# Kernel tuning notes

Measured on AMD Instinct MI355X. Metric: run time of the kernel, lower is better.

## Reference

```python
import jax, jax.numpy as jnp
import numpy as np

N_HEAD, D_MODEL, D_K, D_V = 16, 1024, 64, 64
BIAS_WEIGHT = 1.0
NEG = -10000.0


def setup_inputs() -> dict:
    key = jax.random.key(0)
    ks = jax.random.split(key, 9)
    B, L = 2, 2048
    q = jax.random.normal(ks[0], (B, L, D_MODEL), dtype=jnp.float32)
    k = jax.random.normal(ks[1], (B, L, D_MODEL), dtype=jnp.float32)
    v = jax.random.normal(ks[2], (B, L, D_MODEL), dtype=jnp.float32)
    mask = jax.random.randint(ks[3], (B, L, L), 0, 2, dtype=jnp.int32)
    bias = jax.random.normal(ks[4], (B, L, L), dtype=jnp.float32)
    s = 1.0 / np.sqrt(D_MODEL)
    w_qs = jax.random.uniform(ks[5], (D_MODEL, N_HEAD * D_K), jnp.float32, -s, s)
    w_ks = jax.random.uniform(ks[6], (D_MODEL, N_HEAD * D_K), jnp.float32, -s, s)
    w_vs = jax.random.uniform(ks[7], (D_MODEL, N_HEAD * D_V), jnp.float32, -s, s)
    w_fc = jax.random.uniform(ks[8], (N_HEAD * D_V, D_MODEL), jnp.float32, -s, s)
    return {"q": q, "k": k, "v": v, "mask": mask, "bias": bias,
            "w_qs": w_qs, "w_ks": w_ks, "w_vs": w_vs, "w_fc": w_fc}


def reference(q, k, v, mask, bias, w_qs, w_ks, w_vs, w_fc):
    B, Lq, _ = q.shape
    # project and split heads: [B, H, L, d]
    qh = (q @ w_qs).reshape(B, Lq, N_HEAD, D_K).transpose(0, 2, 1, 3)
    kh = (k @ w_ks).reshape(B, k.shape[1], N_HEAD, D_K).transpose(0, 2, 1, 3)
    vh = (v @ w_vs).reshape(B, v.shape[1], N_HEAD, D_V).transpose(0, 2, 1, 3)
    temperature = D_K ** 0.5
    attn = jnp.einsum('bhqd,bhkd->bhqk', qh / temperature, kh)
    attn = attn + bias[:, None, :, :] * BIAS_WEIGHT
    attn = jnp.where(mask[:, None, :, :] == 0, NEG, attn)
    attn = jax.nn.softmax(attn, axis=-1)
    out = jnp.einsum('bhqk,bhkd->bhqd', attn, vh)
    out = out.transpose(0, 2, 1, 3).reshape(B, Lq, N_HEAD * D_V)
    return out @ w_fc
```

## Files before the change

kernel.cpp:

```cpp
#include <hip/hip_runtime.h>
#include <cstddef>

#define DEV static __device__ __forceinline__

typedef float f32x4 __attribute__((ext_vector_type(4)));
typedef __bf16 bf16x8 __attribute__((ext_vector_type(8)));
typedef __bf16 bf16x4v __attribute__((ext_vector_type(4)));
typedef unsigned short u16x8 __attribute__((ext_vector_type(8)));
typedef unsigned short u16x4 __attribute__((ext_vector_type(4)));
typedef unsigned u32x2 __attribute__((ext_vector_type(2)));
typedef unsigned u32x4 __attribute__((ext_vector_type(4)));
typedef _Float16 f16;
typedef _Float16 f16x4 __attribute__((ext_vector_type(4)));

constexpr int BB = 2, LL = 2048, DM = 1024, NH = 16, DK = 64;
constexpr float LOG2E = 1.44269504f;

DEV unsigned short f2bf(float f) {
  unsigned u = __builtin_bit_cast(unsigned, f);
  u += 0x7fffu + ((u >> 16) & 1u);
  return (unsigned short)(u >> 16);
}
DEV u16x4 cvt4(f32x4 v) {
  bf16x4v b = __builtin_convertvector(v, bf16x4v);
  return __builtin_bit_cast(u16x4, b);
}
DEV bf16x8 asbf(u16x8 v) { return __builtin_bit_cast(bf16x8, v); }
DEV f32x4 mfma16(u16x8 a, u16x8 b, f32x4 c) {
  return __builtin_amdgcn_mfma_f32_16x16x32_bf16(asbf(a), asbf(b), c, 0, 0, 0);
}
#if __has_builtin(__builtin_amdgcn_exp2f)
DEV float fexp2(float x) { return __builtin_amdgcn_exp2f(x); }
#else
DEV float fexp2(float x) { return exp2f(x); }
#endif
DEV void swap32(unsigned& a, unsigned& b) {
#if __has_builtin(__builtin_amdgcn_permlane32_swap)
  u32x2 r = __builtin_amdgcn_permlane32_swap(a, b, false, false);
  a = r[0]; b = r[1];
#else
  asm("v_permlane32_swap_b32 %0, %1" : "+v"(a), "+v"(b));
#endif
}
DEV void swap16(unsigned& a, unsigned& b) {
#if __has_builtin(__builtin_amdgcn_permlane16_swap)
  u32x2 r = __builtin_amdgcn_permlane16_swap(a, b, false, false);
  a = r[0]; b = r[1];
#else
  asm("v_permlane16_swap_b32 %0, %1" : "+v"(a), "+v"(b));
#endif
}
DEV void g2lds16(const void* g, void* l) {
  __builtin_amdgcn_global_load_lds(
      (const __attribute__((address_space(1))) unsigned int*)g,
      (__attribute__((address_space(3))) unsigned int*)l, 16, 0, 0);
}

__global__ __launch_bounds__(256) void prep_all(
    const float* __restrict__ w0, const float* __restrict__ w1,
    const float* __restrict__ w2, const float* __restrict__ w3,
    unsigned short* __restrict__ wT, const int* __restrict__ mask,
    const float* __restrict__ bias, f16* __restrict__ bmf,
    const float* __restrict__ s0, const float* __restrict__ s1,
    const float* __restrict__ s2, unsigned short* __restrict__ qkvb,
    float* __restrict__ dout) {
  int f = blockIdx.x, t = threadIdx.x;
  if (f < 4096) {
    __shared__ float tile[32][33];
    int z = f >> 10, rem = f & 1023;
    int k0 = (rem >> 5) * 32, n0 = (rem & 31) * 32;
    const float* W = (z == 0) ? w0 : (z == 1) ? w1 : (z == 2) ? w2 : w3;
    unsigned short* out = wT + (size_t)z * DM * DM;
    int tx = t & 31, ty = t >> 5;
#pragma unroll
    for (int p = 0; p < 4; p++)
      tile[ty + 8 * p][tx] = W[(size_t)(k0 + ty + 8 * p) * DM + n0 + tx];
    __syncthreads();
#pragma unroll
    for (int p = 0; p < 4; p++)
      out[(size_t)(n0 + ty + 8 * p) * DM + k0 + tx] = f2bf(tile[tx][ty + 8 * p]);
  } else if (f < 12288) {
    int f2 = f - 4096;
    int w = t >> 6, lane = t & 63;
    int bq = f2 >> 5;
    int kt = (f2 & 31) * 4 + w;
    int b = bq >> 7, qt = bq & 127;
    int q = qt * 16 + (lane & 15);
    int k = kt * 16 + (lane >> 4) * 4;
    size_t src = ((size_t)b * LL + q) * LL + k;
    int4 mk = *(const int4*)(mask + src);
    float4 bs = *(const float4*)(bias + src);
    f16x4 o;
    o[0] = (f16)((mk.x == 0 ? -10000.f : bs.x) * LOG2E);
    o[1] = (f16)((mk.y == 0 ? -10000.f : bs.y) * LOG2E);
    o[2] = (f16)((mk.z == 0 ? -10000.f : bs.z) * LOG2E);
    o[3] = (f16)((mk.w == 0 ? -10000.f : bs.w) * LOG2E);
    *(f16x4*)(bmf + ((size_t)bq * 128 + kt) * 256 + lane * 4) = o;
  } else if (f < 18432) {
    int f3 = f - 12288;
    int z = f3 >> 11;
    const float* src = (z == 0) ? s0 : (z == 1) ? s1 : s2;
    size_t i = ((size_t)(f3 & 2047) * 256 + t) * 8;
    float4 a = *(const float4*)(src + i);
    float4 b = *(const float4*)(src + i + 4);
    u16x8 o;
    o[0] = f2bf(a.x); o[1] = f2bf(a.y); o[2] = f2bf(a.z); o[3] = f2bf(a.w);
    o[4] = f2bf(b.x); o[5] = f2bf(b.y); o[6] = f2bf(b.z); o[7] = f2bf(b.w);
    *(u16x8*)(qkvb + (size_t)z * (size_t)(BB * LL) * DM + i) = o;
  } else {
    size_t i = ((size_t)(f - 18432) * 256 + t) * 4;
    float4 zz = {0.f, 0.f, 0.f, 0.f};
    *(float4*)(dout + i) = zz;
  }
}

template <int KITERS>
DEV void gemm_core(const unsigned short* __restrict__ A,
                   const unsigned short* __restrict__ BT,
                   unsigned short* Al, unsigned short* Bl,
                   int m0, int n0, int k0beg, int t, f32x4 (&acc)[4][4]) {
  int lane = t & 63, c = lane & 15, qd = lane >> 4;
  int w = t >> 6, wm = w >> 1, wn = w & 1;
  int r0 = t >> 3;
  int gsw = (t & 7) ^ (r0 & 7);

#pragma unroll 1
  for (int kk = 0; kk < KITERS; ++kk) {
    int k0 = k0beg + kk * 64;
#pragma unroll
    for (int p = 0; p < 4; ++p) {
      g2lds16(&A[(size_t)(m0 + 32 * p + r0) * DM + k0 + 8 * gsw],
              &Al[p * 2048 + w * 512]);
      g2lds16(&BT[(size_t)(n0 + 32 * p + r0) * DM + k0 + 8 * gsw],
              &Bl[p * 2048 + w * 512]);
    }
    __syncthreads();
#pragma unroll
    for (int ks = 0; ks < 2; ++ks) {
      u16x8 af[4], bfr[4];
#pragma unroll
      for (int mt = 0; mt < 4; ++mt)
        af[mt] = *(const u16x8*)&Al[(64 * wm + 16 * mt + c) * 64 +
                                    (((4 * ks + qd) ^ (c & 7)) << 3)];
#pragma unroll
      for (int nt = 0; nt < 4; ++nt)
        bfr[nt] = *(const u16x8*)&Bl[(64 * wn + 16 * nt + c) * 64 +
                                     (((4 * ks + qd) ^ (c & 7)) << 3)];
#pragma unroll
      for (int mt = 0; mt < 4; ++mt)
#pragma unroll
        for (int nt = 0; nt < 4; ++nt)
          acc[mt][nt] = mfma16(af[mt], bfr[nt], acc[mt][nt]);
    }
    __syncthreads();
  }
}

__global__ __launch_bounds__(256, 3) void proj_gemm(
    const unsigned short* __restrict__ qkvb, const unsigned short* __restrict__ wT,
    unsigned short* __restrict__ qh, unsigned short* __restrict__ kh,
    unsigned short* __restrict__ vT) {
  __shared__ unsigned short Al[128 * 64];
  __shared__ unsigned short Bl[128 * 64];
  int z = blockIdx.z;
  const unsigned short* A = qkvb + (size_t)z * BB * LL * DM;
  const unsigned short* BT = wT + (size_t)z * DM * DM;
  int t = threadIdx.x, lane = t & 63, c = lane & 15, qd = lane >> 4;
  int w = t >> 6, wm = w >> 1, wn = w & 1;
  int m0 = blockIdx.y * 128, n0 = blockIdx.x * 128;
  f32x4 acc[4][4] = {};
  gemm_core<DM / 64>(A, BT, Al, Bl, m0, n0, 0, t, acc);

  if (z == 2) {
#pragma unroll
    for (int mt = 0; mt < 4; ++mt)
#pragma unroll
      for (int nt = 0; nt < 4; ++nt) {
        int n = n0 + 64 * wn + 16 * nt + c;
        int h = n >> 6, d = n & 63;
        int m = m0 + 64 * wm + 16 * mt + 4 * qd;
        int b = m >> 11, l = m & 2047;
        *(u16x4*)&vT[(((size_t)b * NH + h) * DK + d) * LL + l] = cvt4(acc[mt][nt]);
      }
  } else {
    unsigned short* Ch = z ? kh : qh;
    float scale = z ? 1.0f : 0.125f * LOG2E;
#pragma unroll
    for (int mt = 0; mt < 4; ++mt)
#pragma unroll
      for (int nt = 0; nt < 4; ++nt) {
        int n = n0 + 64 * wn + 16 * nt + c;
        int h = n >> 6, d = n & 63;
#pragma unroll
        for (int i = 0; i < 4; ++i) {
          int m = m0 + 64 * wm + 16 * mt + 4 * qd + i;
          int b = m >> 11, l = m & 2047;
          Ch[(((size_t)b * NH + h) * LL + l) * DK + d] = f2bf(acc[mt][nt][i] * scale);
        }
      }
  }
}

__global__ __launch_bounds__(256, 3) void fc_gemm(const unsigned short* __restrict__ A,
                                                  const unsigned short* __restrict__ BT,
                                                  float* __restrict__ C) {
  __shared__ unsigned short Al[128 * 64];
  __shared__ unsigned short Bl[128 * 64];
  int t = threadIdx.x, lane = t & 63, c = lane & 15, qd = lane >> 4;
  int w = t >> 6, wm = w >> 1, wn = w & 1;
  int m0 = blockIdx.y * 128, n0 = blockIdx.x * 128;
  f32x4 acc[4][4] = {};
  gemm_core<8>(A, BT, Al, Bl, m0, n0, blockIdx.z * 512, t, acc);
#pragma unroll
  for (int mt = 0; mt < 4; ++mt)
#pragma unroll
    for (int nt = 0; nt < 4; ++nt) {
      int n = n0 + 64 * wn + 16 * nt + c;
#pragma unroll
      for (int i = 0; i < 4; ++i) {
        int m = m0 + 64 * wm + 16 * mt + 4 * qd + i;
        unsafeAtomicAdd(&C[(size_t)m * DM + n], acc[mt][nt][i]);
      }
    }
}

__global__ __launch_bounds__(256, 4) void attn_kern(
    const unsigned short* __restrict__ qh, const unsigned short* __restrict__ kh,
    const unsigned short* __restrict__ vT, const f16* __restrict__ bmf,
    unsigned short* __restrict__ O) {
  __shared__ unsigned short Kb[2][4096];
  __shared__ unsigned short Vb[2][4096];

  int t = threadIdx.x, w = t >> 6, lane = t & 63, c = lane & 15, qd = lane >> 4;
  int q0 = blockIdx.x * 64, h = blockIdx.y, b = blockIdx.z;
  const unsigned short* Q = qh + (((size_t)b * NH + h) * LL + q0) * DK;
  const unsigned short* K = kh + ((size_t)b * NH + h) * LL * DK;
  const unsigned short* V = vT + ((size_t)b * NH + h) * DK * LL;
  const f16* BMF = bmf + (((size_t)b * 128 + blockIdx.x * 4 + w) * 128) * 256 +
                   lane * 4;
  int rt = t >> 3, gg = t & 7;

#pragma unroll
  for (int r = 0; r < 2; ++r) {
    int row = r * 32 + rt;
    int sc = ((gg ^ (row & 7)) << 3);
    g2lds16(&Q[(size_t)row * DK + sc], &Kb[1][r * 2048 + w * 512]);
    g2lds16(&K[(size_t)row * DK + sc], &Kb[0][r * 2048 + w * 512]);
    g2lds16(&V[(size_t)row * LL + sc], &Vb[0][r * 2048 + w * 512]);
  }
  f16x4 bA[4], bB[4];
#pragma unroll
  for (int mt = 0; mt < 4; ++mt) bA[mt] = *(const f16x4*)&BMF[(size_t)mt * 256];
  __syncthreads();

  u16x8 qf[2];
#pragma unroll
  for (int ks = 0; ks < 2; ++ks)
    qf[ks] = *(const u16x8*)&Kb[1][(16 * w + c) * 64 +
                                   (((4 * ks + qd) ^ (c & 7)) << 3)];
  __syncthreads();

  const u16x8 ones = {0x3F80, 0x3F80, 0x3F80, 0x3F80,
                      0x3F80, 0x3F80, 0x3F80, 0x3F80};
  f32x4 lacc = {};
  f32x4 oacc[4] = {};

  auto body = [&](int it, f16x4 (&bc)[4], f16x4 (&bn)[4]) {
    int cur = it & 1;
    const unsigned short* Kl = Kb[cur];
    const unsigned short* Vt = Vb[cur];
    if (it + 1 < 32) {
      int nb = cur ^ 1, kt1 = (it + 1) * 64;
#pragma unroll
      for (int r = 0; r < 2; ++r) {
        int row = r * 32 + rt;
        int sc = ((gg ^ (row & 7)) << 3);
        g2lds16(&K[(size_t)(kt1 + row) * DK + sc], &Kb[nb][r * 2048 + w * 512]);
        g2lds16(&V[(size_t)row * LL + kt1 + sc], &Vb[nb][r * 2048 + w * 512]);
      }
#pragma unroll
      for (int mt = 0; mt < 4; ++mt)
        bn[mt] = *(const f16x4*)&BMF[(size_t)((it + 1) * 4 + mt) * 256];
    }

    f32x4 s[4];
    __builtin_amdgcn_s_setprio(1);
#pragma unroll
    for (int mt = 0; mt < 4; ++mt) {
      int row = 16 * mt + c;
      u16x8 k0f = *(const u16x8*)&Kl[row * 64 + ((qd ^ (c & 7)) << 3)];
      u16x8 k1f = *(const u16x8*)&Kl[row * 64 + (((4 + qd) ^ (c & 7)) << 3)];
      f32x4 z = {0.f, 0.f, 0.f, 0.f};
      z = mfma16(k0f, qf[0], z);
      s[mt] = mfma16(k1f, qf[1], z);
    }
    __builtin_amdgcn_s_setprio(0);
    u16x8 pf[2];
    {
      unsigned L[4], H[4];
#pragma unroll
      for (int mt = 0; mt < 4; ++mt) {
        f16x4 b4 = bc[mt];
        f32x4 p;
#pragma unroll
        for (int i = 0; i < 4; ++i) p[i] = fexp2(s[mt][i] + (float)b4[i]);
        u32x2 lw = __builtin_bit_cast(u32x2, cvt4(p));
        L[mt] = lw[0];
        H[mt] = lw[1];
      }
#pragma unroll
      for (int ks = 0; ks < 2; ++ks) {
        unsigned l0 = L[2 * ks], l1 = L[2 * ks + 1];
        unsigned h0 = H[2 * ks], h1 = H[2 * ks + 1];
        swap32(l0, l1); swap16(l0, l1);
        swap32(h0, h1); swap16(h0, h1);
        u32x4 pw = {l0, h0, l1, h1};
        pf[ks] = __builtin_bit_cast(u16x8, pw);
      }
    }
    __builtin_amdgcn_s_setprio(1);
    lacc = mfma16(ones, pf[0], lacc);
    lacc = mfma16(ones, pf[1], lacc);
#pragma unroll
    for (int dt = 0; dt < 4; ++dt) {
      int row = 16 * dt + c;
      u16x8 v0f = *(const u16x8*)&Vt[row * 64 + ((qd ^ (c & 7)) << 3)];
      u16x8 v1f = *(const u16x8*)&Vt[row * 64 + (((4 + qd) ^ (c & 7)) << 3)];
      oacc[dt] = mfma16(v0f, pf[0], oacc[dt]);
      oacc[dt] = mfma16(v1f, pf[1], oacc[dt]);
    }
    __builtin_amdgcn_s_setprio(0);
    __syncthreads();
  };

#pragma unroll 1
  for (int it = 0; it < 32; it += 2) {
    body(it, bA, bB);
    body(it + 1, bB, bA);
  }

  {
    float rl = 1.f / lacc[0];
    size_t orow = ((size_t)b * LL + q0 + 16 * w + c) * DM + h * DK;
#pragma unroll
    for (int dt = 0; dt < 4; ++dt)
      *(u16x4*)&O[orow + 16 * dt + 4 * qd] = cvt4(oacc[dt] * rl);
  }
}

extern "C" void kernel_launch(void* const* d_in, const int* in_sizes, int n_in,
                              void* d_out, int out_size, void* d_ws, size_t ws_size,
                              hipStream_t stream) {
  (void)in_sizes; (void)n_in; (void)ws_size; (void)out_size;
  const float* q = (const float*)d_in[0];
  const float* k = (const float*)d_in[1];
  const float* v = (const float*)d_in[2];
  const int* mask = (const int*)d_in[3];
  const float* bias = (const float*)d_in[4];
  const float* w_qs = (const float*)d_in[5];
  const float* w_ks = (const float*)d_in[6];
  const float* w_vs = (const float*)d_in[7];
  const float* w_fc = (const float*)d_in[8];

  char* ws = (char*)d_ws;
  const size_t MB = 1024 * 1024;
  unsigned short* wT = (unsigned short*)(ws);
  f16* bmf = (f16*)(ws + 8 * MB);
  unsigned short* qkvb = (unsigned short*)(ws + 24 * MB);
  unsigned short* qh = (unsigned short*)(ws + 48 * MB);
  unsigned short* kh = (unsigned short*)(ws + 56 * MB);
  unsigned short* vhT = (unsigned short*)(ws + 64 * MB);
  unsigned short* Obuf = (unsigned short*)(ws + 72 * MB);

  prep_all<<<dim3(22528), dim3(256), 0, stream>>>(w_qs, w_ks, w_vs, w_fc, wT,
                                                  mask, bias, bmf, q, k, v, qkvb,
                                                  (float*)d_out);
  proj_gemm<<<dim3(8, 32, 3), 256, 0, stream>>>(qkvb, wT, qh, kh, vhT);
  attn_kern<<<dim3(32, 16, 2), 256, 0, stream>>>(qh, kh, vhT, bmf, Obuf);
  fc_gemm<<<dim3(8, 32, 2), 256, 0, stream>>>(Obuf, wT + (size_t)3 * DM * DM,
                                              (float*)d_out);
}
```

Baseline: 294.4 us.

## Drop fc split-K atomics, remap GEMM blocks across XCDs, fold bias into MFMA accumulator

The fc GEMM no longer uses split-K with atomic adds. Each block now covers the full K range and writes its output directly, which also removes the zero-fill of the output in the prep kernel. Both GEMMs use a 1D grid with a block-index remap, likely so that neighbouring tiles land on the same XCD and share L2. In attention, the bias/mask term now seeds the MFMA accumulator instead of being added before exp2, saving some VALU adds. The trade-off is that fc_gemm launches only 256 blocks with twice the K loop, so the machine is less full.

```diff
diff --git a/kernel.cpp b/kernel.cpp
--- a/kernel.cpp
+++ b/kernel.cpp
@@ -62,8 +62,7 @@
     unsigned short* __restrict__ wT, const int* __restrict__ mask,
     const float* __restrict__ bias, f16* __restrict__ bmf,
     const float* __restrict__ s0, const float* __restrict__ s1,
-    const float* __restrict__ s2, unsigned short* __restrict__ qkvb,
-    float* __restrict__ dout) {
+    const float* __restrict__ s2, unsigned short* __restrict__ qkvb) {
   int f = blockIdx.x, t = threadIdx.x;
   if (f < 4096) {
     __shared__ float tile[32][33];
@@ -96,7 +95,7 @@
     o[2] = (f16)((mk.z == 0 ? -10000.f : bs.z) * LOG2E);
     o[3] = (f16)((mk.w == 0 ? -10000.f : bs.w) * LOG2E);
     *(f16x4*)(bmf + ((size_t)bq * 128 + kt) * 256 + lane * 4) = o;
-  } else if (f < 18432) {
+  } else {
     int f3 = f - 12288;
     int z = f3 >> 11;
     const float* src = (z == 0) ? s0 : (z == 1) ? s1 : s2;
@@ -107,10 +106,6 @@
     o[0] = f2bf(a.x); o[1] = f2bf(a.y); o[2] = f2bf(a.z); o[3] = f2bf(a.w);
     o[4] = f2bf(b.x); o[5] = f2bf(b.y); o[6] = f2bf(b.z); o[7] = f2bf(b.w);
     *(u16x8*)(qkvb + (size_t)z * (size_t)(BB * LL) * DM + i) = o;
-  } else {
-    size_t i = ((size_t)(f - 18432) * 256 + t) * 4;
-    float4 zz = {0.f, 0.f, 0.f, 0.f};
-    *(float4*)(dout + i) = zz;
   }
 }
 
@@ -162,12 +157,14 @@
     unsigned short* __restrict__ vT) {
   __shared__ unsigned short Al[128 * 64];
   __shared__ unsigned short Bl[128 * 64];
-  int z = blockIdx.z;
+  int o = blockIdx.x;
+  int wg = (o & 7) * 96 + (o >> 3);
+  int z = wg >> 8, rem = wg & 255;
+  int m0 = (rem >> 3) * 128, n0 = (rem & 7) * 128;
   const unsigned short* A = qkvb + (size_t)z * BB * LL * DM;
   const unsigned short* BT = wT + (size_t)z * DM * DM;
   int t = threadIdx.x, lane = t & 63, c = lane & 15, qd = lane >> 4;
   int w = t >> 6, wm = w >> 1, wn = w & 1;
-  int m0 = blockIdx.y * 128, n0 = blockIdx.x * 128;
   f32x4 acc[4][4] = {};
   gemm_core<DM / 64>(A, BT, Al, Bl, m0, n0, 0, t, acc);
 
@@ -206,11 +203,13 @@
                                                   float* __restrict__ C) {
   __shared__ unsigned short Al[128 * 64];
   __shared__ unsigned short Bl[128 * 64];
+  int o = blockIdx.x;
+  int wg = (o & 7) * 32 + (o >> 3);
+  int m0 = (wg >> 3) * 128, n0 = (wg & 7) * 128;
   int t = threadIdx.x, lane = t & 63, c = lane & 15, qd = lane >> 4;
   int w = t >> 6, wm = w >> 1, wn = w & 1;
-  int m0 = blockIdx.y * 128, n0 = blockIdx.x * 128;
   f32x4 acc[4][4] = {};
-  gemm_core<8>(A, BT, Al, Bl, m0, n0, blockIdx.z * 512, t, acc);
+  gemm_core<DM / 64>(A, BT, Al, Bl, m0, n0, 0, t, acc);
 #pragma unroll
   for (int mt = 0; mt < 4; ++mt)
 #pragma unroll
@@ -219,7 +218,7 @@
 #pragma unroll
       for (int i = 0; i < 4; ++i) {
         int m = m0 + 64 * wm + 16 * mt + 4 * qd + i;
-        unsafeAtomicAdd(&C[(size_t)m * DM + n], acc[mt][nt][i]);
+        C[(size_t)m * DM + n] = acc[mt][nt][i];
       }
     }
 }
@@ -290,7 +289,8 @@
       int row = 16 * mt + c;
       u16x8 k0f = *(const u16x8*)&Kl[row * 64 + ((qd ^ (c & 7)) << 3)];
       u16x8 k1f = *(const u16x8*)&Kl[row * 64 + (((4 + qd) ^ (c & 7)) << 3)];
-      f32x4 z = {0.f, 0.f, 0.f, 0.f};
+      f16x4 b4 = bc[mt];
+      f32x4 z = {(float)b4[0], (float)b4[1], (float)b4[2], (float)b4[3]};
       z = mfma16(k0f, qf[0], z);
       s[mt] = mfma16(k1f, qf[1], z);
     }
@@ -300,10 +300,9 @@
       unsigned L[4], H[4];
 #pragma unroll
       for (int mt = 0; mt < 4; ++mt) {
-        f16x4 b4 = bc[mt];
         f32x4 p;
 #pragma unroll
-        for (int i = 0; i < 4; ++i) p[i] = fexp2(s[mt][i] + (float)b4[i]);
+        for (int i = 0; i < 4; ++i) p[i] = fexp2(s[mt][i]);
         u32x2 lw = __builtin_bit_cast(u32x2, cvt4(p));
         L[mt] = lw[0];
         H[mt] = lw[1];
@@ -372,11 +371,10 @@
   unsigned short* vhT = (unsigned short*)(ws + 64 * MB);
   unsigned short* Obuf = (unsigned short*)(ws + 72 * MB);
 
-  prep_all<<<dim3(22528), dim3(256), 0, stream>>>(w_qs, w_ks, w_vs, w_fc, wT,
-                                                  mask, bias, bmf, q, k, v, qkvb,
-                                                  (float*)d_out);
-  proj_gemm<<<dim3(8, 32, 3), 256, 0, stream>>>(qkvb, wT, qh, kh, vhT);
+  prep_all<<<dim3(18432), dim3(256), 0, stream>>>(w_qs, w_ks, w_vs, w_fc, wT,
+                                                  mask, bias, bmf, q, k, v, qkvb);
+  proj_gemm<<<dim3(768), 256, 0, stream>>>(qkvb, wT, qh, kh, vhT);
   attn_kern<<<dim3(32, 16, 2), 256, 0, stream>>>(qh, kh, vhT, bmf, Obuf);
-  fc_gemm<<<dim3(8, 32, 2), 256, 0, stream>>>(Obuf, wT + (size_t)3 * DM * DM,
-                                              (float*)d_out);
-}
+  fc_gemm<<<dim3(256), 256, 0, stream>>>(Obuf, wT + (size_t)3 * DM * DM,
+                                         (float*)d_out);
+}
```

New measurement: 267.5 us. -9.1%, faster.
